# Kernel optimization log

Hardware: AMD Instinct MI355X
Metric: run time of the kernel (lower is better)

Reference implementation:

```python
import jax, jax.numpy as jnp
import numpy as np

IN_DIM = 96
HIDDEN = 256
EPS = 1e-6
NEG = -1e10


def setup_inputs() -> dict:
    key = jax.random.key(0)
    ks = jax.random.split(key, 12)
    B, S = 8, 2048
    q = jax.random.normal(ks[0], (B, S, IN_DIM), dtype=jnp.float32)
    k = jax.random.normal(ks[1], (B, S, IN_DIM), dtype=jnp.float32)
    v = jax.random.normal(ks[2], (B, S, IN_DIM), dtype=jnp.float32)
    mask = jax.random.randint(ks[3], (B, S, S), 0, 2, dtype=jnp.int32)
    s = 1.0 / np.sqrt(IN_DIM)
    Wq = jax.random.normal(ks[4], (IN_DIM, HIDDEN), dtype=jnp.float32) * s
    bq = jax.random.normal(ks[5], (HIDDEN,), dtype=jnp.float32) * 0.01
    Wk = jax.random.normal(ks[6], (IN_DIM, HIDDEN), dtype=jnp.float32) * s
    bk = jax.random.normal(ks[7], (HIDDEN,), dtype=jnp.float32) * 0.01
    Wv = jax.random.normal(ks[8], (IN_DIM, HIDDEN), dtype=jnp.float32) * s
    bv = jax.random.normal(ks[9], (HIDDEN,), dtype=jnp.float32) * 0.01
    gamma = jnp.ones((HIDDEN,), dtype=jnp.float32)
    beta = jnp.zeros((HIDDEN,), dtype=jnp.float32)
    return {"query": q, "key": k, "value": v, "mask": mask,
            "Wq": Wq, "bq": bq, "Wk": Wk, "bk": bk, "Wv": Wv, "bv": bv,
            "gamma": gamma, "beta": beta}


def reference(query, key, value, mask, Wq, bq, Wk, bk, Wv, bv, gamma, beta):
    # Linear projections: [B,S,96] @ [96,H] -> [B,S,H]
    q = jnp.einsum('bsf,fh->bsh', query, Wq) + bq
    k = jnp.einsum('bsf,fh->bsh', key, Wk) + bk
    v = jnp.einsum('bsf,fh->bsh', value, Wv) + bv
    # Scaled dot-product scores: [B,S,S]
    score = jnp.einsum('bqh,bkh->bqk', q, k) / jnp.sqrt(jnp.float32(HIDDEN))
    score = jnp.where(mask == 0, jnp.float32(NEG), score)
    attn = jax.nn.softmax(score, axis=-1)
    out = jnp.einsum('bqk,bkh->bqh', attn, v)
    # LayerNorm over last dim, eps=1e-6
    mu = jnp.mean(out, axis=-1, keepdims=True)
    var = jnp.mean(jnp.square(out - mu), axis=-1, keepdims=True)
    normed = (out - mu) * jax.lax.rsqrt(var + EPS)
    return normed * gamma + beta
```

## Files before the change

kernel.cpp:

```cpp
#include <hip/hip_runtime.h>

#define B_   8
#define S_   2048
#define IN_  96
#define H_   256

typedef float f32x4 __attribute__((ext_vector_type(4)));
typedef short bf16x8 __attribute__((ext_vector_type(8)));

__device__ __forceinline__ unsigned short f2bf(float x) {
    unsigned int u = __float_as_uint(x);
    u += 0x7fffu + ((u >> 16) & 1u);
    return (unsigned short)(u >> 16);
}

__global__ __launch_bounds__(256) void wconv_kernel(
    const float* __restrict__ Wq, const float* __restrict__ Wk,
    const float* __restrict__ Wv, unsigned short* __restrict__ wt)
{
    const int p  = blockIdx.x >> 3;
    const int h0 = (blockIdx.x & 7) * 32;
    const float* W = (p == 0) ? Wq : (p == 1) ? Wk : Wv;
    unsigned short* dst = wt + (size_t)p * H_ * IN_ + (size_t)h0 * IN_;

    __shared__ unsigned short lds[32][100];
    const int t = threadIdx.x;
    #pragma unroll
    for (int i = 0; i < 12; ++i) {
        int idx = i * 256 + t;
        int f = idx >> 5;
        int hl = idx & 31;
        lds[hl][f] = f2bf(W[f * H_ + h0 + hl]);
    }
    __syncthreads();
    #pragma unroll
    for (int j = 0; j < 6; ++j) {
        int e = (j * 256 + t) * 2;
        int hl = e / IN_, f = e % IN_;
        unsigned int pk = (unsigned int)lds[hl][f] |
                          ((unsigned int)lds[hl][f + 1] << 16);
        ((unsigned int*)dst)[j * 256 + t] = pk;
    }
}

__global__ __launch_bounds__(256) void proj_kernel3(
    const float* __restrict__ query, const float* __restrict__ key,
    const float* __restrict__ value, const unsigned short* __restrict__ wt,
    const float* __restrict__ bq, const float* __restrict__ bk,
    const float* __restrict__ bv,
    unsigned short* __restrict__ pq, unsigned short* __restrict__ pk,
    unsigned short* __restrict__ pv)
{
    __shared__ unsigned short Xs[3][16][104];

    const int t    = threadIdx.x;
    const int lane = t & 63;
    const int wave = t >> 6;
    const int col  = lane & 15;
    const int quad = lane >> 4;
    const int bi   = blockIdx.x;
    const int s0   = bi * 16;
    const int b    = s0 >> 11;
    const int sl   = s0 & (S_ - 1);

    const float* srcs[3] = { query + (size_t)s0 * IN_,
                             key   + (size_t)s0 * IN_,
                             value + (size_t)s0 * IN_ };
    #pragma unroll
    for (int p = 0; p < 3; ++p) {
        #pragma unroll
        for (int i = 0; i < 2; ++i) {
            int idx = i * 256 + t;
            if (idx < 384) {
                f32x4 x = *(const f32x4*)(srcs[p] + idx * 4);
                int r = idx / 24;
                int f = (idx - r * 24) * 4;
                unsigned long long pkk =
                    (unsigned long long)f2bf(x[0])
                  | ((unsigned long long)f2bf(x[1]) << 16)
                  | ((unsigned long long)f2bf(x[2]) << 32)
                  | ((unsigned long long)f2bf(x[3]) << 48);
                *(unsigned long long*)&Xs[p][r][f] = pkk;
            }
        }
    }
    __syncthreads();

    const int hc = wave;
    #pragma unroll
    for (int p = 0; p < 3; ++p) {
        const unsigned short* wbase = wt + (size_t)p * H_ * IN_;
        bf16x8 wfr[4][3];
        #pragma unroll
        for (int ht = 0; ht < 4; ++ht)
            #pragma unroll
            for (int kc = 0; kc < 3; ++kc)
                wfr[ht][kc] = *(const bf16x8*)(wbase
                    + (size_t)(hc * 64 + ht * 16 + col) * IN_ + kc * 32 + quad * 8);
        bf16x8 xfr[3];
        #pragma unroll
        for (int kc = 0; kc < 3; ++kc)
            xfr[kc] = *(const bf16x8*)&Xs[p][col][kc * 32 + quad * 8];

        f32x4 acc[4];
        #pragma unroll
        for (int ht = 0; ht < 4; ++ht) acc[ht] = (f32x4)(0.0f);
        #pragma unroll
        for (int kc = 0; kc < 3; ++kc)
            #pragma unroll
            for (int ht = 0; ht < 4; ++ht)
                acc[ht] = (p < 2)
                    ? __builtin_amdgcn_mfma_f32_16x16x32_bf16(xfr[kc], wfr[ht][kc], acc[ht], 0, 0, 0)
                    : __builtin_amdgcn_mfma_f32_16x16x32_bf16(wfr[ht][kc], xfr[kc], acc[ht], 0, 0, 0);

        if (p < 2) {
            unsigned short* dst  = (p == 0) ? pq : pk;
            const float*    bias = (p == 0) ? bq : bk;
            #pragma unroll
            for (int ht = 0; ht < 4; ++ht) {
                float bh = bias[hc * 64 + ht * 16 + col];
                const int s    = hc * 2 + (ht >> 1);
                const int lq   = ((ht & 1) * 2 + (col >> 3)) * 16;
                const int j    = col & 7;
                #pragma unroll
                for (int r = 0; r < 4; ++r)
                    dst[(size_t)(((bi * 8 + s) * 64 + lq + quad * 4 + r)) * 8 + j]
                        = f2bf(acc[ht][r] + bh);
            }
        } else {
            const int kl  = (sl & 63) + col;
            const int c   = sl >> 6;
            const int s2  = kl >> 5;
            const int qv  = (kl >> 3) & 3;
            const int jj  = col & 7;
            #pragma unroll
            for (int ht = 0; ht < 4; ++ht) {
                f32x4 b4 = *(const f32x4*)(bv + hc * 64 + ht * 16 + quad * 4);
                #pragma unroll
                for (int r = 0; r < 4; ++r)
                    pv[(size_t)(((b * 32 + c) * 32 + hc * 8 + ht * 2 + s2) * 64
                                + qv * 16 + quad * 4 + r) * 8 + jj]
                        = f2bf(acc[ht][r] + b4[r]);
            }
        }
    }
}

__global__ __launch_bounds__(256, 3) void attn_kernel(
    const unsigned short* __restrict__ pq, const unsigned short* __restrict__ pk,
    const unsigned short* __restrict__ pv, const int* __restrict__ mask,
    const float* __restrict__ gamma, const float* __restrict__ beta,
    float* __restrict__ out)
{
    __shared__ union {
        unsigned short P[2][16][72];
        float Obuf[16][260];
    } sm;
    __shared__ float lsum[4][16];

    const int tid  = threadIdx.x;
    const int wave = tid >> 6;
    const int lane = tid & 63;
    const int col  = lane & 15;
    const int quad = lane >> 4;

    const int b     = blockIdx.x & 7;
    const int strip = blockIdx.x >> 3;
    const int q0    = strip << 4;
    const int tq    = b * 128 + strip;

    const unsigned short* qb = pq + (size_t)tq * 8 * 64 * 8 + lane * 8;
    bf16x8 qf[8];
    #pragma unroll
    for (int s = 0; s < 8; ++s) qf[s] = *(const bf16x8*)(qb + s * 512);

    f32x4 O[4];
    #pragma unroll
    for (int ht = 0; ht < 4; ++ht) O[ht] = (f32x4)(0.0f);
    float l = 0.0f;

    const unsigned short* pkb = pk + (size_t)(b * 128) * 8 * 512 + lane * 8;
    const unsigned short* pvb = pv + (size_t)(b * 32) * 32 * 512
                                   + (size_t)wave * 8 * 512 + lane * 8;
    const int* mbase = mask + (size_t)(b * S_ + q0 + col) * S_ + wave * 16 + quad * 4;

    int4 mcur, mnext;
    mcur = *(const int4*)(mbase);

    #pragma unroll 2
    for (int c = 0; c < 32; ++c) {
        const int pb = c & 1;

        if (c < 31) mnext = *(const int4*)(mbase + (c + 1) * 64);

        const unsigned short* kb = pkb + (size_t)(c * 4 + wave) * 8 * 512;
        bf16x8 kf[8];
        #pragma unroll
        for (int s = 0; s < 8; ++s) kf[s] = *(const bf16x8*)(kb + s * 512);
        f32x4 St = (f32x4)(0.0f);
        #pragma unroll
        for (int s = 0; s < 8; ++s)
            St = __builtin_amdgcn_mfma_f32_16x16x32_bf16(kf[s], qf[s], St, 0, 0, 0);

        const unsigned short* vb = pvb + (size_t)c * 32 * 512;
        bf16x8 vf[4][2];
        #pragma unroll
        for (int ht = 0; ht < 4; ++ht)
            #pragma unroll
            for (int s2 = 0; s2 < 2; ++s2)
                vf[ht][s2] = *(const bf16x8*)(vb + (size_t)(ht * 2 + s2) * 512);

        {
            int mi[4] = { mcur.x, mcur.y, mcur.z, mcur.w };
            unsigned long long pk64 = 0;
            #pragma unroll
            for (int r = 0; r < 4; ++r) {
                float p = (mi[r] == 0) ? 0.0f
                        : __expf(St[r] * 0.0625f - 6.0f);
                l += p;
                pk64 |= (unsigned long long)f2bf(p) << (16 * r);
            }
            *(unsigned long long*)&sm.P[pb][col][wave * 16 + quad * 4] = pk64;
        }
        mcur = mnext;

        __syncthreads();

        #pragma unroll
        for (int s2 = 0; s2 < 2; ++s2) {
            bf16x8 pf = *(const bf16x8*)&sm.P[pb][col][s2 * 32 + quad * 8];
            #pragma unroll
            for (int ht = 0; ht < 4; ++ht)
                O[ht] = __builtin_amdgcn_mfma_f32_16x16x32_bf16(pf, vf[ht][s2], O[ht], 0, 0, 0);
        }
    }

    l += __shfl_xor(l, 16);
    l += __shfl_xor(l, 32);
    if (lane < 16) lsum[wave][lane] = l;
    __syncthreads();

    float ltot = lsum[0][col] + lsum[1][col] + lsum[2][col] + lsum[3][col];
    float linv = 1.0f / ltot;
    float li4[4];
    #pragma unroll
    for (int r = 0; r < 4; ++r) li4[r] = __shfl(linv, quad * 4 + r);

    #pragma unroll
    for (int ht = 0; ht < 4; ++ht)
        #pragma unroll
        for (int r = 0; r < 4; ++r)
            sm.Obuf[quad * 4 + r][wave * 64 + ht * 16 + col] = O[ht][r] * li4[r];
    __syncthreads();

    {
        const int q = tid >> 4;
        const int i = tid & 15;
        float vals[16];
        float sum = 0.0f;
        #pragma unroll
        for (int j = 0; j < 16; ++j) {
            vals[j] = sm.Obuf[q][j * 16 + i];
            sum += vals[j];
        }
        sum += __shfl_xor(sum, 1);
        sum += __shfl_xor(sum, 2);
        sum += __shfl_xor(sum, 4);
        sum += __shfl_xor(sum, 8);
        float mu = sum * (1.0f / H_);
        float sq = 0.0f;
        #pragma unroll
        for (int j = 0; j < 16; ++j) {
            float d = vals[j] - mu;
            sq += d * d;
        }
        sq += __shfl_xor(sq, 1);
        sq += __shfl_xor(sq, 2);
        sq += __shfl_xor(sq, 4);
        sq += __shfl_xor(sq, 8);
        float rstd = rsqrtf(sq * (1.0f / H_) + 1e-6f);

        float* orow = out + (size_t)(b * S_ + q0 + q) * H_;
        #pragma unroll
        for (int j = 0; j < 16; ++j) {
            int h = j * 16 + i;
            orow[h] = (vals[j] - mu) * rstd * gamma[h] + beta[h];
        }
    }
}

extern "C" void kernel_launch(void* const* d_in, const int* in_sizes, int n_in,
                              void* d_out, int out_size, void* d_ws, size_t ws_size,
                              hipStream_t stream)
{
    const float* query = (const float*)d_in[0];
    const float* key   = (const float*)d_in[1];
    const float* value = (const float*)d_in[2];
    const int*   mask  = (const int*)d_in[3];
    const float* Wq = (const float*)d_in[4];
    const float* bq = (const float*)d_in[5];
    const float* Wk = (const float*)d_in[6];
    const float* bk = (const float*)d_in[7];
    const float* Wv = (const float*)d_in[8];
    const float* bv = (const float*)d_in[9];
    const float* gamma = (const float*)d_in[10];
    const float* beta  = (const float*)d_in[11];
    float* out = (float*)d_out;

    const size_t NQK = (size_t)B_ * S_ * H_;
    unsigned short* pq = (unsigned short*)d_ws;
    unsigned short* pk = pq + NQK;
    unsigned short* pv = pk + NQK;
    unsigned short* wt = pv + NQK;

    wconv_kernel<<<24, 256, 0, stream>>>(Wq, Wk, Wv, wt);
    proj_kernel3<<<B_ * S_ / 16, 256, 0, stream>>>(query, key, value, wt,
                                                   bq, bk, bv, pq, pk, pv);
    attn_kernel<<<B_ * S_ / 16, 256, 0, stream>>>(pq, pk, pv, mask, gamma, beta, out);
}
```

Before: 344.6 us.

## Switch to fp16 MFMA and process two query strips per attention block

Replaces bf16 with fp16 for projections and attention MFMAs, and doubles the query rows per attention block (32 instead of 16), so each K/V tile loaded from global memory is reused across two query strips. K fragments are double-buffered in registers and prefetched one chunk ahead, and the grid is halved with launch bounds lowered to 2 blocks per CU. This cuts K/V global traffic per query row and hides K load latency, at the cost of more registers and lower occupancy. Using fp16 for probabilities and projections risks overflow or precision change relative to bf16, since fp16 has a much smaller exponent range.

```diff
diff --git a/kernel.cpp b/kernel.cpp
--- a/kernel.cpp
+++ b/kernel.cpp
@@ -5,13 +5,11 @@
 #define IN_  96
 #define H_   256
 
-typedef float f32x4 __attribute__((ext_vector_type(4)));
-typedef short bf16x8 __attribute__((ext_vector_type(8)));
-
-__device__ __forceinline__ unsigned short f2bf(float x) {
-    unsigned int u = __float_as_uint(x);
-    u += 0x7fffu + ((u >> 16) & 1u);
-    return (unsigned short)(u >> 16);
+typedef float    f32x4 __attribute__((ext_vector_type(4)));
+typedef _Float16 f16x8 __attribute__((ext_vector_type(8)));
+
+__device__ __forceinline__ unsigned short f2h(float x) {
+    return __builtin_bit_cast(unsigned short, (_Float16)x);
 }
 
 __global__ __launch_bounds__(256) void wconv_kernel(
@@ -30,7 +28,7 @@
         int idx = i * 256 + t;
         int f = idx >> 5;
         int hl = idx & 31;
-        lds[hl][f] = f2bf(W[f * H_ + h0 + hl]);
+        lds[hl][f] = f2h(W[f * H_ + h0 + hl]);
     }
     __syncthreads();
     #pragma unroll
@@ -76,10 +74,10 @@
                 int r = idx / 24;
                 int f = (idx - r * 24) * 4;
                 unsigned long long pkk =
-                    (unsigned long long)f2bf(x[0])
-                  | ((unsigned long long)f2bf(x[1]) << 16)
-                  | ((unsigned long long)f2bf(x[2]) << 32)
-                  | ((unsigned long long)f2bf(x[3]) << 48);
+                    (unsigned long long)f2h(x[0])
+                  | ((unsigned long long)f2h(x[1]) << 16)
+                  | ((unsigned long long)f2h(x[2]) << 32)
+                  | ((unsigned long long)f2h(x[3]) << 48);
                 *(unsigned long long*)&Xs[p][r][f] = pkk;
             }
         }
@@ -90,17 +88,17 @@
     #pragma unroll
     for (int p = 0; p < 3; ++p) {
         const unsigned short* wbase = wt + (size_t)p * H_ * IN_;
-        bf16x8 wfr[4][3];
+        f16x8 wfr[4][3];
         #pragma unroll
         for (int ht = 0; ht < 4; ++ht)
             #pragma unroll
             for (int kc = 0; kc < 3; ++kc)
-                wfr[ht][kc] = *(const bf16x8*)(wbase
+                wfr[ht][kc] = *(const f16x8*)(wbase
                     + (size_t)(hc * 64 + ht * 16 + col) * IN_ + kc * 32 + quad * 8);
-        bf16x8 xfr[3];
+        f16x8 xfr[3];
         #pragma unroll
         for (int kc = 0; kc < 3; ++kc)
-            xfr[kc] = *(const bf16x8*)&Xs[p][col][kc * 32 + quad * 8];
+            xfr[kc] = *(const f16x8*)&Xs[p][col][kc * 32 + quad * 8];
 
         f32x4 acc[4];
         #pragma unroll
@@ -110,8 +108,8 @@
             #pragma unroll
             for (int ht = 0; ht < 4; ++ht)
                 acc[ht] = (p < 2)
-                    ? __builtin_amdgcn_mfma_f32_16x16x32_bf16(xfr[kc], wfr[ht][kc], acc[ht], 0, 0, 0)
-                    : __builtin_amdgcn_mfma_f32_16x16x32_bf16(wfr[ht][kc], xfr[kc], acc[ht], 0, 0, 0);
+                    ? __builtin_amdgcn_mfma_f32_16x16x32_f16(xfr[kc], wfr[ht][kc], acc[ht], 0, 0, 0)
+                    : __builtin_amdgcn_mfma_f32_16x16x32_f16(wfr[ht][kc], xfr[kc], acc[ht], 0, 0, 0);
 
         if (p < 2) {
             unsigned short* dst  = (p == 0) ? pq : pk;
@@ -125,7 +123,7 @@
                 #pragma unroll
                 for (int r = 0; r < 4; ++r)
                     dst[(size_t)(((bi * 8 + s) * 64 + lq + quad * 4 + r)) * 8 + j]
-                        = f2bf(acc[ht][r] + bh);
+                        = f2h(acc[ht][r] + bh);
             }
         } else {
             const int kl  = (sl & 63) + col;
@@ -140,23 +138,23 @@
                 for (int r = 0; r < 4; ++r)
                     pv[(size_t)(((b * 32 + c) * 32 + hc * 8 + ht * 2 + s2) * 64
                                 + qv * 16 + quad * 4 + r) * 8 + jj]
-                        = f2bf(acc[ht][r] + b4[r]);
-            }
-        }
-    }
-}
-
-__global__ __launch_bounds__(256, 3) void attn_kernel(
+                        = f2h(acc[ht][r] + b4[r]);
+            }
+        }
+    }
+}
+
+__global__ __launch_bounds__(256, 2) void attn_kernel(
     const unsigned short* __restrict__ pq, const unsigned short* __restrict__ pk,
     const unsigned short* __restrict__ pv, const int* __restrict__ mask,
     const float* __restrict__ gamma, const float* __restrict__ beta,
     float* __restrict__ out)
 {
     __shared__ union {
-        unsigned short P[2][16][72];
-        float Obuf[16][260];
+        unsigned short P[2][32][68];
+        float Obuf[32][260];
     } sm;
-    __shared__ float lsum[4][16];
+    __shared__ float lsum[4][32];
 
     const int tid  = threadIdx.x;
     const int wave = tid >> 6;
@@ -166,95 +164,139 @@
 
     const int b     = blockIdx.x & 7;
     const int strip = blockIdx.x >> 3;
-    const int q0    = strip << 4;
-    const int tq    = b * 128 + strip;
-
-    const unsigned short* qb = pq + (size_t)tq * 8 * 64 * 8 + lane * 8;
-    bf16x8 qf[8];
-    #pragma unroll
-    for (int s = 0; s < 8; ++s) qf[s] = *(const bf16x8*)(qb + s * 512);
-
-    f32x4 O[4];
-    #pragma unroll
-    for (int ht = 0; ht < 4; ++ht) O[ht] = (f32x4)(0.0f);
-    float l = 0.0f;
-
-    const unsigned short* pkb = pk + (size_t)(b * 128) * 8 * 512 + lane * 8;
+    const int q0    = strip << 5;
+
+    f16x8 qf[2][8];
+    #pragma unroll
+    for (int st = 0; st < 2; ++st) {
+        const unsigned short* qb = pq + (size_t)(b * 128 + strip * 2 + st) * 4096
+                                      + lane * 8;
+        #pragma unroll
+        for (int s = 0; s < 8; ++s) qf[st][s] = *(const f16x8*)(qb + s * 512);
+    }
+
+    f32x4 O[2][4];
+    #pragma unroll
+    for (int st = 0; st < 2; ++st)
+        #pragma unroll
+        for (int ht = 0; ht < 4; ++ht) O[st][ht] = (f32x4)(0.0f);
+    float l0 = 0.0f, l1 = 0.0f;
+
+    const unsigned short* pkb = pk + (size_t)(b * 128) * 4096 + lane * 8;
     const unsigned short* pvb = pv + (size_t)(b * 32) * 32 * 512
                                    + (size_t)wave * 8 * 512 + lane * 8;
-    const int* mbase = mask + (size_t)(b * S_ + q0 + col) * S_ + wave * 16 + quad * 4;
-
-    int4 mcur, mnext;
-    mcur = *(const int4*)(mbase);
+    const int* mb0 = mask + (size_t)(b * S_ + q0 + col) * S_ + wave * 16 + quad * 4;
+    const int* mb1 = mb0 + 16 * S_;
+
+    f16x8 kf[2][8];
+    #pragma unroll
+    for (int s = 0; s < 8; ++s)
+        kf[0][s] = *(const f16x8*)(pkb + (size_t)wave * 4096 + s * 512);
+
+    int4 mc0 = *(const int4*)mb0;
+    int4 mc1 = *(const int4*)mb1;
 
     #pragma unroll 2
     for (int c = 0; c < 32; ++c) {
         const int pb = c & 1;
-
-        if (c < 31) mnext = *(const int4*)(mbase + (c + 1) * 64);
-
-        const unsigned short* kb = pkb + (size_t)(c * 4 + wave) * 8 * 512;
-        bf16x8 kf[8];
-        #pragma unroll
-        for (int s = 0; s < 8; ++s) kf[s] = *(const bf16x8*)(kb + s * 512);
-        f32x4 St = (f32x4)(0.0f);
-        #pragma unroll
-        for (int s = 0; s < 8; ++s)
-            St = __builtin_amdgcn_mfma_f32_16x16x32_bf16(kf[s], qf[s], St, 0, 0, 0);
+        const int cn = (c < 31) ? c + 1 : c;
 
         const unsigned short* vb = pvb + (size_t)c * 32 * 512;
-        bf16x8 vf[4][2];
+        f16x8 vf[4][2];
         #pragma unroll
         for (int ht = 0; ht < 4; ++ht)
             #pragma unroll
             for (int s2 = 0; s2 < 2; ++s2)
-                vf[ht][s2] = *(const bf16x8*)(vb + (size_t)(ht * 2 + s2) * 512);
+                vf[ht][s2] = *(const f16x8*)(vb + (size_t)(ht * 2 + s2) * 512);
+
+        int4 mn0 = *(const int4*)(mb0 + cn * 64);
+        int4 mn1 = *(const int4*)(mb1 + cn * 64);
+
+        f32x4 St0 = (f32x4)(0.0f), St1 = (f32x4)(0.0f);
+        #pragma unroll
+        for (int s = 0; s < 8; ++s) {
+            St0 = __builtin_amdgcn_mfma_f32_16x16x32_f16(kf[pb][s], qf[0][s], St0, 0, 0, 0);
+            St1 = __builtin_amdgcn_mfma_f32_16x16x32_f16(kf[pb][s], qf[1][s], St1, 0, 0, 0);
+        }
 
         {
-            int mi[4] = { mcur.x, mcur.y, mcur.z, mcur.w };
+            const unsigned short* kb = pkb + (size_t)(cn * 4 + wave) * 4096;
+            #pragma unroll
+            for (int s = 0; s < 8; ++s)
+                kf[pb ^ 1][s] = *(const f16x8*)(kb + s * 512);
+        }
+
+        {
+            int mi[4] = { mc0.x, mc0.y, mc0.z, mc0.w };
             unsigned long long pk64 = 0;
             #pragma unroll
             for (int r = 0; r < 4; ++r) {
-                float p = (mi[r] == 0) ? 0.0f
-                        : __expf(St[r] * 0.0625f - 6.0f);
-                l += p;
-                pk64 |= (unsigned long long)f2bf(p) << (16 * r);
+                float p = (mi[r] == 0) ? 0.0f : __expf(St0[r] * 0.0625f - 6.0f);
+                _Float16 ph = (_Float16)p;
+                l0 += (float)ph;
+                pk64 |= (unsigned long long)__builtin_bit_cast(unsigned short, ph)
+                        << (16 * r);
             }
             *(unsigned long long*)&sm.P[pb][col][wave * 16 + quad * 4] = pk64;
         }
-        mcur = mnext;
+        {
+            int mi[4] = { mc1.x, mc1.y, mc1.z, mc1.w };
+            unsigned long long pk64 = 0;
+            #pragma unroll
+            for (int r = 0; r < 4; ++r) {
+                float p = (mi[r] == 0) ? 0.0f : __expf(St1[r] * 0.0625f - 6.0f);
+                _Float16 ph = (_Float16)p;
+                l1 += (float)ph;
+                pk64 |= (unsigned long long)__builtin_bit_cast(unsigned short, ph)
+                        << (16 * r);
+            }
+            *(unsigned long long*)&sm.P[pb][16 + col][wave * 16 + quad * 4] = pk64;
+        }
+        mc0 = mn0; mc1 = mn1;
 
         __syncthreads();
 
         #pragma unroll
-        for (int s2 = 0; s2 < 2; ++s2) {
-            bf16x8 pf = *(const bf16x8*)&sm.P[pb][col][s2 * 32 + quad * 8];
-            #pragma unroll
-            for (int ht = 0; ht < 4; ++ht)
-                O[ht] = __builtin_amdgcn_mfma_f32_16x16x32_bf16(pf, vf[ht][s2], O[ht], 0, 0, 0);
-        }
-    }
-
-    l += __shfl_xor(l, 16);
-    l += __shfl_xor(l, 32);
-    if (lane < 16) lsum[wave][lane] = l;
+        for (int st = 0; st < 2; ++st) {
+            #pragma unroll
+            for (int s2 = 0; s2 < 2; ++s2) {
+                union { unsigned long long u[2]; f16x8 v; } pu;
+                const unsigned short* pr = &sm.P[pb][st * 16 + col][s2 * 32 + quad * 8];
+                pu.u[0] = *(const unsigned long long*)pr;
+                pu.u[1] = *(const unsigned long long*)(pr + 4);
+                f16x8 pf = pu.v;
+                #pragma unroll
+                for (int ht = 0; ht < 4; ++ht)
+                    O[st][ht] = __builtin_amdgcn_mfma_f32_16x16x32_f16(pf, vf[ht][s2], O[st][ht], 0, 0, 0);
+            }
+        }
+    }
+
+    l0 += __shfl_xor(l0, 16); l0 += __shfl_xor(l0, 32);
+    l1 += __shfl_xor(l1, 16); l1 += __shfl_xor(l1, 32);
+    if (lane < 16) { lsum[wave][lane] = l0; lsum[wave][16 + lane] = l1; }
     __syncthreads();
 
-    float ltot = lsum[0][col] + lsum[1][col] + lsum[2][col] + lsum[3][col];
-    float linv = 1.0f / ltot;
-    float li4[4];
-    #pragma unroll
-    for (int r = 0; r < 4; ++r) li4[r] = __shfl(linv, quad * 4 + r);
-
-    #pragma unroll
-    for (int ht = 0; ht < 4; ++ht)
-        #pragma unroll
-        for (int r = 0; r < 4; ++r)
-            sm.Obuf[quad * 4 + r][wave * 64 + ht * 16 + col] = O[ht][r] * li4[r];
+    #pragma unroll
+    for (int st = 0; st < 2; ++st) {
+        float ltot = lsum[0][st * 16 + col] + lsum[1][st * 16 + col]
+                   + lsum[2][st * 16 + col] + lsum[3][st * 16 + col];
+        float linv = 1.0f / ltot;
+        float li4[4];
+        #pragma unroll
+        for (int r = 0; r < 4; ++r) li4[r] = __shfl(linv, quad * 4 + r);
+        #pragma unroll
+        for (int ht = 0; ht < 4; ++ht)
+            #pragma unroll
+            for (int r = 0; r < 4; ++r)
+                sm.Obuf[st * 16 + quad * 4 + r][wave * 64 + ht * 16 + col]
+                    = O[st][ht][r] * li4[r];
+    }
     __syncthreads();
 
-    {
-        const int q = tid >> 4;
+    #pragma unroll
+    for (int st = 0; st < 2; ++st) {
+        const int q = st * 16 + (tid >> 4);
         const int i = tid & 15;
         float vals[16];
         float sum = 0.0f;
@@ -316,5 +358,5 @@
     wconv_kernel<<<24, 256, 0, stream>>>(Wq, Wk, Wv, wt);
     proj_kernel3<<<B_ * S_ / 16, 256, 0, stream>>>(query, key, value, wt,
                                                    bq, bk, bv, pq, pk, pv);
-    attn_kernel<<<B_ * S_ / 16, 256, 0, stream>>>(pq, pk, pv, mask, gamma, beta, out);
-}
+    attn_kernel<<<B_ * S_ / 32, 256, 0, stream>>>(pq, pk, pv, mask, gamma, beta, out);
+}
```

After: 304.4 us. 11.6% less time.
